# Kernel tuning notes

Measured on AMD Instinct MI355X. Metric: run time of the kernel, lower is better.

Reference implementation:

```python
import jax, jax.numpy as jnp
import numpy as np

N = 50000
E = 800000
IN_CH = 128
HID = 64
H1 = 4  # heads in gat1
NEG_SLOPE = 0.2


def _gat_layer(x, src, dst, W, a_src, a_dst, bias, heads, ch):
    # x: [N, F_in]; W: [F_in, heads*ch]; a_src/a_dst: [heads, ch]; bias: [heads*ch]
    n = x.shape[0]
    h = (x @ W).reshape(n, heads, ch)                       # [N, H, C]
    alpha_src = jnp.einsum('nhc,hc->nh', h, a_src)          # [N, H]
    alpha_dst = jnp.einsum('nhc,hc->nh', h, a_dst)          # [N, H]
    e = jax.nn.leaky_relu(alpha_src[src] + alpha_dst[dst], NEG_SLOPE)  # [E, H]
    # segment softmax over incoming edges of each destination node
    m = jax.ops.segment_max(e, dst, num_segments=n)         # [N, H]
    ex = jnp.exp(e - m[dst])                                # [E, H]
    denom = jax.ops.segment_sum(ex, dst, num_segments=n)    # [N, H]
    alpha = ex / (denom[dst] + 1e-16)                       # [E, H]
    out = jax.ops.segment_sum(alpha[:, :, None] * h[src], dst, num_segments=n)  # [N, H, C]
    return out.reshape(n, heads * ch) + bias


def setup_inputs() -> dict:
    key = jax.random.key(0)
    ks = jax.random.split(key, 12)
    x = jax.random.normal(ks[0], (N, IN_CH), dtype=jnp.float32)
    edge_index = jax.random.randint(ks[1], (2, E), 0, N, dtype=jnp.int64)
    s1 = 1.0 / np.sqrt(IN_CH)
    s2 = 1.0 / np.sqrt(H1 * HID)
    s3 = 1.0 / np.sqrt(HID)
    return {
        'x': x,
        'edge_index': edge_index,
        'W1': jax.random.uniform(ks[2], (IN_CH, H1 * HID), jnp.float32, -s1, s1),
        'att_src1': jax.random.uniform(ks[3], (H1, HID), jnp.float32, -s1, s1),
        'att_dst1': jax.random.uniform(ks[4], (H1, HID), jnp.float32, -s1, s1),
        'b1': jnp.zeros((H1 * HID,), jnp.float32),
        'W2': jax.random.uniform(ks[5], (H1 * HID, HID), jnp.float32, -s2, s2),
        'att_src2': jax.random.uniform(ks[6], (1, HID), jnp.float32, -s2, s2),
        'att_dst2': jax.random.uniform(ks[7], (1, HID), jnp.float32, -s2, s2),
        'b2': jnp.zeros((HID,), jnp.float32),
        'W_out': jax.random.uniform(ks[8], (HID, 1), jnp.float32, -s3, s3),
        'b_out': jnp.zeros((1,), jnp.float32),
    }


def reference(x, edge_index, W1, att_src1, att_dst1, b1, W2, att_src2, att_dst2, b2, W_out, b_out):
    # add self-loops (PyG GATConv default)
    loops = jnp.arange(N, dtype=edge_index.dtype)
    src = jnp.concatenate([edge_index[0], loops])
    dst = jnp.concatenate([edge_index[1], loops])
    h = jax.nn.relu(_gat_layer(x, src, dst, W1, att_src1, att_dst1, b1, H1, HID))
    h = jax.nn.relu(_gat_layer(h, src, dst, W2, att_src2, att_dst2, b2, 1, HID))
    return (h @ W_out + b_out).squeeze(-1)  # [N]
```

## Files before the change

kernel.cpp:

```cpp
#include <hip/hip_runtime.h>
#include <hip/hip_bf16.h>
#include <math.h>

#define N_NODES 50000
#define N_EDGES 800000
#define EE_TOTAL (N_EDGES + N_NODES)
#define CAP 64

#define GEMM1_BLOCKS ((N_NODES + 63) / 64)
#define EPB 1088

typedef __attribute__((ext_vector_type(8))) short bf16x8;
typedef __attribute__((ext_vector_type(4))) float f32x4;

__device__ __forceinline__ float bf2f(unsigned short s) {
  return __uint_as_float((unsigned)s << 16);
}
__device__ __forceinline__ unsigned short f2bf(float f) {
  unsigned u = __float_as_uint(f);
  return (unsigned short)((u + 0x7FFFu + ((u >> 16) & 1u)) >> 16);
}
__device__ __forceinline__ float lrelu(float e) { return e > 0.f ? e : 0.2f * e; }

__global__ void prep_kernel(const float* __restrict__ W1, const float* __restrict__ W2,
                            unsigned short* __restrict__ W1t, unsigned short* __restrict__ W2t,
                            int* __restrict__ counts) {
  int i = blockIdx.x * blockDim.x + threadIdx.x;
  if (i < N_NODES) counts[i] = 0;
  if (i < 256 * 128) W1t[i] = f2bf(W1[(i & 127) * 256 + (i >> 7)]);
  if (i < 64 * 256) W2t[i] = f2bf(W2[(i & 255) * 64 + (i >> 8)]);
}

__global__ __launch_bounds__(256) void fused_kernel(const int* __restrict__ src,
                                                    const int* __restrict__ dst,
                                                    int* __restrict__ counts,
                                                    int* __restrict__ col,
                                                    const float* __restrict__ A,
                                                    const unsigned short* __restrict__ Bt,
                                                    unsigned short* __restrict__ Cb,
                                                    const float* __restrict__ att_s,
                                                    const float* __restrict__ att_d,
                                                    float* __restrict__ as_out,
                                                    float* __restrict__ ad_out) {
  __shared__ unsigned short Bs[256 * 128];
  int id = blockIdx.x;
  int t = threadIdx.x;

  {
    int ebase = id * EPB;
    int elim = min(ebase + EPB, EE_TOTAL);
#pragma unroll
    for (int k = 0; k < 5; ++k) {
      int i = ebase + k * 256 + t;
      if (i < elim) {
        int s_, d_;
        if (i < N_EDGES) { s_ = src[i]; d_ = dst[i]; }
        else { s_ = i - N_EDGES; d_ = s_; }
        int pos = atomicAdd(&counts[d_], 1);
        if (pos < CAP) col[(size_t)d_ * CAP + pos] = s_;
      }
    }
  }

  const int M = N_NODES;
  int lane = t & 63, w = t >> 6;
  int row0 = id * 64;
#pragma unroll
  for (int i = 0; i < 16; ++i) {
    int idx = i * 256 + t;
    int n = idx >> 4;
    uint4 v = ((const uint4*)Bt)[idx];
    int byte = (idx * 16) ^ ((n & 7) << 4);
    *(uint4*)((char*)Bs + byte) = v;
  }
  __syncthreads();
  int rl = lane & 15, kg = lane >> 4;
  f32x4 acc[4][4] = {};
  for (int ks = 0; ks < 4; ++ks) {
    bf16x8 af[4], bfr[4];
#pragma unroll
    for (int rb = 0; rb < 4; ++rb) {
      int row = row0 + rb * 16 + rl;
      float4 v0 = make_float4(0.f, 0.f, 0.f, 0.f), v1 = v0;
      if (row < M) {
        const float* p = A + (size_t)row * 128 + ks * 32 + kg * 8;
        v0 = *(const float4*)p;
        v1 = *(const float4*)(p + 4);
      }
      bf16x8 a;
      a[0] = (short)f2bf(v0.x); a[1] = (short)f2bf(v0.y);
      a[2] = (short)f2bf(v0.z); a[3] = (short)f2bf(v0.w);
      a[4] = (short)f2bf(v1.x); a[5] = (short)f2bf(v1.y);
      a[6] = (short)f2bf(v1.z); a[7] = (short)f2bf(v1.w);
      af[rb] = a;
    }
#pragma unroll
    for (int cb = 0; cb < 4; ++cb) {
      int n = w * 64 + cb * 16 + rl;
      int byte = (n * 256 + ks * 64 + kg * 16) ^ ((n & 7) << 4);
      bfr[cb] = *(const bf16x8*)((char*)Bs + byte);
    }
#pragma unroll
    for (int rb = 0; rb < 4; ++rb)
#pragma unroll
      for (int cb = 0; cb < 4; ++cb)
        acc[rb][cb] = __builtin_amdgcn_mfma_f32_16x16x32_bf16(af[rb], bfr[cb], acc[rb][cb], 0, 0, 0);
  }
  float asv[4], adv[4];
#pragma unroll
  for (int cb = 0; cb < 4; ++cb) {
    int c = w * 64 + cb * 16 + rl;
    asv[cb] = att_s[c];
    adv[cb] = att_d[c];
  }
#pragma unroll
  for (int rb = 0; rb < 4; ++rb) {
#pragma unroll
    for (int r = 0; r < 4; ++r) {
      int row = row0 + rb * 16 + kg * 4 + r;
      bool ok = row < M;
      float sp = 0.f, dp = 0.f;
#pragma unroll
      for (int cb = 0; cb < 4; ++cb) {
        float v = acc[rb][cb][r];
        if (ok) Cb[(size_t)row * 256 + w * 64 + cb * 16 + rl] = f2bf(v);
        sp += v * asv[cb];
        dp += v * adv[cb];
      }
#pragma unroll
      for (int off = 1; off < 16; off <<= 1) {
        sp += __shfl_xor(sp, off, 64);
        dp += __shfl_xor(dp, off, 64);
      }
      if (ok && rl == 0) {
        as_out[row * 4 + w] = sp;
        ad_out[row * 4 + w] = dp;
      }
    }
  }
}

__global__ __launch_bounds__(256) void gemm2_kernel(const unsigned short* __restrict__ A,
                                                    const unsigned short* __restrict__ Bt,
                                                    unsigned short* __restrict__ Cb,
                                                    const float* __restrict__ att_s,
                                                    const float* __restrict__ att_d,
                                                    float* __restrict__ as_out,
                                                    float* __restrict__ ad_out) {
  __shared__ unsigned short Bs[64 * 256];
  const int M = N_NODES;
  int t = threadIdx.x;
  int lane = t & 63, w = t >> 6;
  int row0 = blockIdx.x * 64;
#pragma unroll
  for (int i = 0; i < 8; ++i) {
    int idx = i * 256 + t;
    int n = idx >> 5;
    uint4 v = ((const uint4*)Bt)[idx];
    int byte = (idx * 16) ^ ((n & 7) << 4);
    *(uint4*)((char*)Bs + byte) = v;
  }
  __syncthreads();
  int rl = lane & 15, kg = lane >> 4;
  int arow = row0 + w * 16 + rl;
  f32x4 acc[4] = {};
  for (int ks = 0; ks < 8; ++ks) {
    bf16x8 a = {};
    if (arow < M) a = *(const bf16x8*)(A + (size_t)arow * 256 + ks * 32 + kg * 8);
#pragma unroll
    for (int cb = 0; cb < 4; ++cb) {
      int n = cb * 16 + rl;
      int byte = (n * 512 + ks * 64 + kg * 16) ^ ((n & 7) << 4);
      bf16x8 bfrag = *(const bf16x8*)((char*)Bs + byte);
      acc[cb] = __builtin_amdgcn_mfma_f32_16x16x32_bf16(a, bfrag, acc[cb], 0, 0, 0);
    }
  }
  float asv[4], adv[4];
#pragma unroll
  for (int cb = 0; cb < 4; ++cb) {
    int c = cb * 16 + rl;
    asv[cb] = att_s[c];
    adv[cb] = att_d[c];
  }
#pragma unroll
  for (int r = 0; r < 4; ++r) {
    int orow = row0 + w * 16 + kg * 4 + r;
    bool ok = orow < M;
    float sp = 0.f, dp = 0.f;
#pragma unroll
    for (int cb = 0; cb < 4; ++cb) {
      float v = acc[cb][r];
      if (ok) Cb[(size_t)orow * 64 + cb * 16 + rl] = f2bf(v);
      sp += v * asv[cb];
      dp += v * adv[cb];
    }
#pragma unroll
    for (int off = 1; off < 16; off <<= 1) {
      sp += __shfl_xor(sp, off, 64);
      dp += __shfl_xor(dp, off, 64);
    }
    if (ok && rl == 0) {
      as_out[orow] = sp;
      ad_out[orow] = dp;
    }
  }
}

__global__ __launch_bounds__(256) void agg1_kernel(const unsigned short* __restrict__ h1b,
                                                   const float* __restrict__ as,
                                                   const float* __restrict__ ad,
                                                   const int* __restrict__ counts,
                                                   const int* __restrict__ col,
                                                   const float* __restrict__ b1,
                                                   unsigned short* __restrict__ x2b) {
  __shared__ int s_lds[4][64];
  __shared__ float p_lds[4][64][4];
  int t = threadIdx.x;
  int lane = t & 63, w = t >> 6;
  int node = blockIdx.x * 4 + w;
  if (node >= N_NODES) return;
  int cnt = min(counts[node], CAP);
  const int* cbase = col + (size_t)node * CAP;
  float4 adn = *(const float4*)(ad + node * 4);
  int half = lane >> 5, sl = lane & 31, hd = sl >> 3;
  int s = node;
  float4 p = make_float4(0.f, 0.f, 0.f, 0.f);
  if (lane < cnt) {
    s = cbase[lane];
    float4 a4 = *(const float4*)(as + s * 4);
    p.x = __expf(lrelu(a4.x + adn.x));
    p.y = __expf(lrelu(a4.y + adn.y));
    p.z = __expf(lrelu(a4.z + adn.z));
    p.w = __expf(lrelu(a4.w + adn.w));
  }
  s_lds[w][lane] = s;
  *(float4*)&p_lds[w][lane][0] = p;
  float4 den = p;
#pragma unroll
  for (int off = 1; off < 64; off <<= 1) {
    den.x += __shfl_xor(den.x, off, 64);
    den.y += __shfl_xor(den.y, off, 64);
    den.z += __shfl_xor(den.z, off, 64);
    den.w += __shfl_xor(den.w, off, 64);
  }
  float acc[8] = {};
  int nq = (cnt + 3) & ~3;
  for (int j = 0; j < nq; j += 4) {
    int e0 = j + half, e1 = j + 2 + half;
    int s0 = s_lds[w][e0], s1 = s_lds[w][e1];
    float p0 = p_lds[w][e0][hd], p1 = p_lds[w][e1][hd];
    bf16x8 v0 = *(const bf16x8*)(h1b + (size_t)s0 * 256 + sl * 8);
    bf16x8 v1 = *(const bf16x8*)(h1b + (size_t)s1 * 256 + sl * 8);
#pragma unroll
    for (int k = 0; k < 8; ++k) {
      acc[k] += p0 * bf2f((unsigned short)v0[k]);
      acc[k] += p1 * bf2f((unsigned short)v1[k]);
    }
  }
#pragma unroll
  for (int k = 0; k < 8; ++k) acc[k] += __shfl_xor(acc[k], 32, 64);
  if (half == 0) {
    float dh = (hd == 0) ? den.x : (hd == 1) ? den.y : (hd == 2) ? den.z : den.w;
    float inv = 1.f / (dh + 1e-16f);
    int ch = sl * 8;
    float4 blo = *(const float4*)(b1 + ch);
    float4 bhi = *(const float4*)(b1 + ch + 4);
    float bb[8] = {blo.x, blo.y, blo.z, blo.w, bhi.x, bhi.y, bhi.z, bhi.w};
    bf16x8 o;
#pragma unroll
    for (int k = 0; k < 8; ++k) o[k] = (short)f2bf(fmaxf(acc[k] * inv + bb[k], 0.f));
    *(bf16x8*)(x2b + (size_t)node * 256 + ch) = o;
  }
}

__global__ __launch_bounds__(256) void agg2_final_kernel(const unsigned short* __restrict__ h2b,
                                                         const float* __restrict__ as,
                                                         const float* __restrict__ ad,
                                                         const int* __restrict__ counts,
                                                         const int* __restrict__ col,
                                                         const float* __restrict__ b2,
                                                         const float* __restrict__ Wout,
                                                         const float* __restrict__ bout,
                                                         float* __restrict__ out) {
  __shared__ int s_lds[4][64];
  __shared__ float p_lds[4][64];
  int t = threadIdx.x;
  int lane = t & 63, w = t >> 6;
  int node = blockIdx.x * 4 + w;
  if (node >= N_NODES) return;
  int cnt = min(counts[node], CAP);
  const int* cbase = col + (size_t)node * CAP;
  float adn = ad[node];
  int g = lane >> 4, sl = lane & 15;
  int s = node;
  float p = 0.f;
  if (lane < cnt) {
    s = cbase[lane];
    p = __expf(lrelu(as[s] + adn));
  }
  s_lds[w][lane] = s;
  p_lds[w][lane] = p;
  float den = p;
#pragma unroll
  for (int off = 1; off < 64; off <<= 1) den += __shfl_xor(den, off, 64);
  float acc[4] = {};
  int nq = (cnt + 7) & ~7;
  for (int j = 0; j < nq; j += 8) {
    int e0 = j + g, e1 = j + 4 + g;
    int s0 = s_lds[w][e0], s1 = s_lds[w][e1];
    float p0 = p_lds[w][e0], p1 = p_lds[w][e1];
    ushort4 v0 = *(const ushort4*)(h2b + (size_t)s0 * 64 + sl * 4);
    ushort4 v1 = *(const ushort4*)(h2b + (size_t)s1 * 64 + sl * 4);
    acc[0] += p0 * bf2f(v0.x) + p1 * bf2f(v1.x);
    acc[1] += p0 * bf2f(v0.y) + p1 * bf2f(v1.y);
    acc[2] += p0 * bf2f(v0.z) + p1 * bf2f(v1.z);
    acc[3] += p0 * bf2f(v0.w) + p1 * bf2f(v1.w);
  }
#pragma unroll
  for (int k = 0; k < 4; ++k) {
    acc[k] += __shfl_xor(acc[k], 16, 64);
    acc[k] += __shfl_xor(acc[k], 32, 64);
  }
  float inv = 1.f / (den + 1e-16f);
  int ch = sl * 4;
  float4 b4 = *(const float4*)(b2 + ch);
  float4 w4 = *(const float4*)(Wout + ch);
  float part = fmaxf(acc[0] * inv + b4.x, 0.f) * w4.x +
               fmaxf(acc[1] * inv + b4.y, 0.f) * w4.y +
               fmaxf(acc[2] * inv + b4.z, 0.f) * w4.z +
               fmaxf(acc[3] * inv + b4.w, 0.f) * w4.w;
#pragma unroll
  for (int off = 1; off < 16; off <<= 1) part += __shfl_xor(part, off, 64);
  if (lane == 0) out[node] = part + bout[0];
}

extern "C" void kernel_launch(void* const* d_in, const int* in_sizes, int n_in,
                              void* d_out, int out_size, void* d_ws, size_t ws_size,
                              hipStream_t stream) {
  const float* x    = (const float*)d_in[0];
  const int*   ei   = (const int*)d_in[1];
  const float* W1   = (const float*)d_in[2];
  const float* as1w = (const float*)d_in[3];
  const float* ad1w = (const float*)d_in[4];
  const float* b1   = (const float*)d_in[5];
  const float* W2   = (const float*)d_in[6];
  const float* as2w = (const float*)d_in[7];
  const float* ad2w = (const float*)d_in[8];
  const float* b2   = (const float*)d_in[9];
  const float* Wout = (const float*)d_in[10];
  const float* bout = (const float*)d_in[11];
  float* out = (float*)d_out;

  const int* src = ei;
  const int* dst = ei + N_EDGES;

  char* ws = (char*)d_ws;
  size_t off = 0;
  auto alloc = [&](size_t bytes) -> char* {
    char* p = ws + off;
    off += (bytes + 255) & ~(size_t)255;
    return p;
  };
  int*            counts = (int*)alloc((size_t)N_NODES * 4);
  int*            col    = (int*)alloc((size_t)N_NODES * CAP * 4);
  unsigned short* W1t    = (unsigned short*)alloc((size_t)256 * 128 * 2);
  unsigned short* W2t    = (unsigned short*)alloc((size_t)64 * 256 * 2);
  unsigned short* x2b    = (unsigned short*)alloc((size_t)N_NODES * 256 * 2);
  unsigned short* hbuf   = (unsigned short*)alloc((size_t)N_NODES * 256 * 2);
  float*          as1    = (float*)alloc((size_t)N_NODES * 4 * 4);
  float*          ad1    = (float*)alloc((size_t)N_NODES * 4 * 4);
  float*          as2    = (float*)alloc((size_t)N_NODES * 4);
  float*          ad2    = (float*)alloc((size_t)N_NODES * 4);

  unsigned short* h1b = hbuf;
  unsigned short* h2b = hbuf;

  const int node_blocks4 = (N_NODES + 3) / 4;
  const int gemm_blocks = (N_NODES + 63) / 64;

  prep_kernel<<<(N_NODES + 255) / 256, 256, 0, stream>>>(W1, W2, W1t, W2t, counts);

  fused_kernel<<<GEMM1_BLOCKS, 256, 0, stream>>>(src, dst, counts, col,
                                                 x, W1t, h1b, as1w, ad1w, as1, ad1);

  agg1_kernel<<<node_blocks4, 256, 0, stream>>>(h1b, as1, ad1, counts, col, b1, x2b);

  gemm2_kernel<<<gemm_blocks, 256, 0, stream>>>(x2b, W2t, h2b, as2w, ad2w, as2, ad2);
  agg2_final_kernel<<<node_blocks4, 256, 0, stream>>>(h2b, as2, ad2, counts, col, b2,
                                                      Wout, bout, out);
}
```

Measured before the change: 177.4 us.

## Split edge scatter from GEMM1 and partition scatter by destination range

Moves the CSR-style edge bucketing out of the fused GEMM1 kernel into its own kernel. Each block handles one edge chunk and one of 8 destination-node ranges, so atomics and col writes from concurrent blocks target a narrower node range, for better cache locality of counts and col. The cost is that every edge index is read 8 times, plus an extra kernel launch, and the overlap of scatter with GEMM work that the fused kernel provided is lost.

```diff
diff --git a/kernel.cpp b/kernel.cpp
--- a/kernel.cpp
+++ b/kernel.cpp
@@ -6,9 +6,9 @@
 #define N_EDGES 800000
 #define EE_TOTAL (N_EDGES + N_NODES)
 #define CAP 64
-
-#define GEMM1_BLOCKS ((N_NODES + 63) / 64)
-#define EPB 1088
+#define NRANGE 6250
+#define SC_CHUNK 2048
+#define SC_CHUNKS ((EE_TOTAL + SC_CHUNK - 1) / SC_CHUNK)
 
 typedef __attribute__((ext_vector_type(8))) short bf16x8;
 typedef __attribute__((ext_vector_type(4))) float f32x4;
@@ -31,11 +31,30 @@
   if (i < 64 * 256) W2t[i] = f2bf(W2[(i & 255) * 64 + (i >> 8)]);
 }
 
-__global__ __launch_bounds__(256) void fused_kernel(const int* __restrict__ src,
-                                                    const int* __restrict__ dst,
-                                                    int* __restrict__ counts,
-                                                    int* __restrict__ col,
-                                                    const float* __restrict__ A,
+__global__ __launch_bounds__(256) void scatter_kernel(const int* __restrict__ src,
+                                                      const int* __restrict__ dst,
+                                                      int* __restrict__ counts,
+                                                      int* __restrict__ col) {
+  int range = blockIdx.x & 7;
+  int chunk = blockIdx.x >> 3;
+  int lo = range * NRANGE, hi = lo + NRANGE;
+  int base = chunk * SC_CHUNK + threadIdx.x;
+#pragma unroll
+  for (int k = 0; k < SC_CHUNK / 256; ++k) {
+    int i = base + k * 256;
+    if (i < EE_TOTAL) {
+      int s, d;
+      if (i < N_EDGES) { s = src[i]; d = dst[i]; }
+      else { s = i - N_EDGES; d = s; }
+      if (d >= lo && d < hi) {
+        int pos = atomicAdd(&counts[d], 1);
+        if (pos < CAP) col[(size_t)d * CAP + pos] = s;
+      }
+    }
+  }
+}
+
+__global__ __launch_bounds__(256) void gemm1_kernel(const float* __restrict__ A,
                                                     const unsigned short* __restrict__ Bt,
                                                     unsigned short* __restrict__ Cb,
                                                     const float* __restrict__ att_s,
@@ -45,23 +64,6 @@
   __shared__ unsigned short Bs[256 * 128];
   int id = blockIdx.x;
   int t = threadIdx.x;
-
-  {
-    int ebase = id * EPB;
-    int elim = min(ebase + EPB, EE_TOTAL);
-#pragma unroll
-    for (int k = 0; k < 5; ++k) {
-      int i = ebase + k * 256 + t;
-      if (i < elim) {
-        int s_, d_;
-        if (i < N_EDGES) { s_ = src[i]; d_ = dst[i]; }
-        else { s_ = i - N_EDGES; d_ = s_; }
-        int pos = atomicAdd(&counts[d_], 1);
-        if (pos < CAP) col[(size_t)d_ * CAP + pos] = s_;
-      }
-    }
-  }
-
   const int M = N_NODES;
   int lane = t & 63, w = t >> 6;
   int row0 = id * 64;
@@ -380,8 +382,9 @@
 
   prep_kernel<<<(N_NODES + 255) / 256, 256, 0, stream>>>(W1, W2, W1t, W2t, counts);
 
-  fused_kernel<<<GEMM1_BLOCKS, 256, 0, stream>>>(src, dst, counts, col,
-                                                 x, W1t, h1b, as1w, ad1w, as1, ad1);
+  scatter_kernel<<<SC_CHUNKS * 8, 256, 0, stream>>>(src, dst, counts, col);
+
+  gemm1_kernel<<<gemm_blocks, 256, 0, stream>>>(x, W1t, h1b, as1w, ad1w, as1, ad1);
 
   agg1_kernel<<<node_blocks4, 256, 0, stream>>>(h1b, as1, ad1, counts, col, b1, x2b);
 
```

Measured after the change: 175.3 us. No clear change (-1.2%).
